# Kernel tuning notes

Measured on AMD Instinct MI355X. Metric: run time of the kernel, lower is better.

The kernel has to match this reference:

```python
import jax, jax.numpy as jnp
import numpy as np

H = 16  # n_heads

def setup_inputs() -> dict:
    key = jax.random.key(0)
    k1, k2, k3, k4 = jax.random.split(key, 4)
    B, S, D = 2, 2048, 1024
    query = jax.random.normal(k1, (B, S, D), dtype=jnp.float32)
    pos_emb = jax.random.normal(k2, (S, D), dtype=jnp.float32)
    w_qkv = jax.random.normal(k3, (D, 3 * D), dtype=jnp.float32) * (D ** -0.5)
    w_out = jax.random.normal(k4, (D, D), dtype=jnp.float32) * (D ** -0.5)
    return {"query": query, "pos_emb": pos_emb, "w_qkv": w_qkv, "w_out": w_out}

def reference(query, pos_emb, w_qkv, w_out):
    B, S, D = query.shape
    d_k = D // H
    # ape=True: pos_fn applied to input before QKV projection (additive APE)
    x = query + pos_emb[None, :, :]
    # fused QKV projection; torch view(B,S,H,3*d_k) + chunk(3,-1) == reshape(B,S,H,3,d_k)
    qkv = jnp.einsum('bsd,de->bse', x, w_qkv).reshape(B, S, H, 3, d_k)
    qkv = jnp.transpose(qkv, (0, 2, 1, 3, 4))  # [B,H,S,3,d_k]
    q, k, v = qkv[..., 0, :], qkv[..., 1, :], qkv[..., 2, :]
    scale = d_k ** -0.5
    scores = jnp.einsum('bhqd,bhkd->bhqk', q, k) * scale  # [B,H,S,S]
    attn = jax.nn.softmax(scores, axis=-1)  # dropout is identity in eval
    o = jnp.einsum('bhqk,bhkd->bhqd', attn, v)
    o = jnp.transpose(o, (0, 2, 1, 3)).reshape(B, S, D)
    return jnp.einsum('bsd,de->bse', o, w_out)
```

## Files before the change

kernel.cpp:

```cpp
#include <hip/hip_runtime.h>

#define SS 2048
#define DD 1024
#define N3 3072

typedef unsigned short u16;
typedef unsigned int u32;
typedef __attribute__((ext_vector_type(8))) short bf16x8;
typedef __attribute__((ext_vector_type(4))) short bf16x4;
typedef __attribute__((ext_vector_type(4))) float f32x4;

__device__ __forceinline__ u16 f2bf(float f) {
    u32 u = __float_as_uint(f);
    u32 r = u + 0x7fffu + ((u >> 16) & 1u);
    return (u16)(r >> 16);
}

__device__ __forceinline__ float fast_exp2(float x) {
    return __builtin_amdgcn_exp2f(x);
}

__device__ __forceinline__ void async_cp16(u16* lds, const u16* g) {
    __builtin_amdgcn_global_load_lds((const __attribute__((address_space(1))) u32*)g,
                                     (__attribute__((address_space(3))) u32*)lds, 16, 0, 0);
}

__device__ __forceinline__ f32x4 mfma16(bf16x4 a, bf16x4 b, f32x4 c) {
    return __builtin_amdgcn_mfma_f32_16x16x16bf16_1k(a, b, c, 0, 0, 0);
}

__global__ __launch_bounds__(256)
void prep_all(const float* __restrict__ q, const float* __restrict__ pos,
              const float* __restrict__ wqkv, const float* __restrict__ wout,
              u16* __restrict__ x, u16* __restrict__ wqkvT, u16* __restrict__ woutT)
{
    __shared__ float t[32][33];
    const int bx = blockIdx.x;

    if (bx < 4096) {
        const size_t i = ((size_t)bx * 256 + threadIdx.x) * 4;
        float4 a = *(const float4*)(q + i);
        float4 p = *(const float4*)(pos + (i & (size_t)(SS * DD - 1)));
        uint2 r;
        r.x = (u32)f2bf(a.x + p.x) | ((u32)f2bf(a.y + p.y) << 16);
        r.y = (u32)f2bf(a.z + p.z) | ((u32)f2bf(a.w + p.w) << 16);
        *(uint2*)(x + i) = r;
        return;
    }

    const int isq = bx < 7168;
    const int tt  = isq ? (bx - 4096) : (bx - 7168);
    const int nx  = isq ? 96 : 32;
    const int N   = isq ? N3 : DD;
    const float* W = isq ? wqkv : wout;
    u16* WT = isq ? wqkvT : woutT;

    const int x0 = (tt % nx) * 32, y0 = (tt / nx) * 32;
    const int tx = threadIdx.x & 31, ty = threadIdx.x >> 5;
#pragma unroll
    for (int i = 0; i < 4; ++i)
        t[ty + i * 8][tx] = W[(size_t)(y0 + ty + i * 8) * N + x0 + tx];
    __syncthreads();
#pragma unroll
    for (int i = 0; i < 4; ++i) {
        const int n = x0 + ty + i * 8;
        int dst = n;
        if (isq) {
            const int hh = n / 192, r = n % 192;
            dst = (r < 64) ? hh * 64 + r
                : (r < 128) ? 1024 + hh * 64 + (r - 64)
                            : 2048 + hh * 64 + (r - 128);
        }
        float v = t[tx][ty + i * 8];
        if (isq && dst < 1024) v *= 0.18033688f;
        WT[(size_t)dst * DD + y0 + tx] = f2bf(v);
    }
}

__global__ __launch_bounds__(512, 2)
void gemm256(const u16* __restrict__ A, const u16* __restrict__ BT,
             u16* __restrict__ C, u16* __restrict__ vt, int M, int N, int K, int nbx)
{
    extern __shared__ __align__(16) u16 smem[];

    const int bid = blockIdx.x;
    const int chunk = (int)gridDim.x >> 3;
    const int swz = (bid & 7) * chunk + (bid >> 3);
    const int bxs = swz % nbx, bys = swz / nbx;

    const int tid = threadIdx.x;
    const int lane = tid & 63;
    const int wv = tid >> 6;
    const int quad = lane >> 4, l16 = lane & 15;
    const int wm = wv >> 2, wn = wv & 3;
    const int m0 = bys * 256, n0 = bxs * 256;
    const int sw = l16 & 7;

    const int srow = tid >> 3, pc = tid & 7, lc = pc ^ (srow & 7);
    const u16* agp = A  + (size_t)(m0 + srow) * K + lc * 8;
    const u16* bgp = BT + (size_t)(n0 + srow) * K + lc * 8;
    u16* const asw = smem +         srow * 64 + pc * 8;
    u16* const bsw = smem + 32768 + srow * 64 + pc * 8;

    auto stage = [&](int buf, int k0) {
#pragma unroll
        for (int s = 0; s < 4; ++s)
            async_cp16(asw + buf * 16384 + s * 4096, agp + (size_t)(s * 64) * K + k0);
#pragma unroll
        for (int s = 0; s < 4; ++s)
            async_cp16(bsw + buf * 16384 + s * 4096, bgp + (size_t)(s * 64) * K + k0);
    };

    f32x4 acc[8][4];
#pragma unroll
    for (int i = 0; i < 8; ++i)
#pragma unroll
        for (int j = 0; j < 4; ++j) acc[i][j] = {0.f, 0.f, 0.f, 0.f};

    stage(0, 0);

    const int NT = K / 64;
    for (int t = 0; t < NT; ++t) {
        const int p = t & 1;
        asm volatile("s_waitcnt vmcnt(0) lgkmcnt(0)\n\ts_barrier" ::: "memory");
        if (t + 1 < NT) stage(p ^ 1, (t + 1) * 64);

        const u16* Ab = smem +         p * 16384;
        const u16* Bb = smem + 32768 + p * 16384;

#pragma unroll
        for (int ks = 0; ks < 2; ++ks) {
            bf16x8 bfr[4];
#pragma unroll
            for (int nt = 0; nt < 4; ++nt)
                bfr[nt] = *(const bf16x8*)&Bb[(wn * 64 + nt * 16 + l16) * 64 + (((ks * 4 + quad) ^ sw) << 3)];
#pragma unroll
            for (int mt = 0; mt < 8; ++mt) {
                bf16x8 af = *(const bf16x8*)&Ab[(wm * 128 + mt * 16 + l16) * 64 + (((ks * 4 + quad) ^ sw) << 3)];
#pragma unroll
                for (int nt = 0; nt < 4; ++nt)
                    acc[mt][nt] = __builtin_amdgcn_mfma_f32_16x16x32_bf16(af, bfr[nt], acc[mt][nt], 0, 0, 0);
            }
        }
    }

    if (vt && n0 >= 2048) {
        __syncthreads();
        u16* tb = smem;
#pragma unroll
        for (int mt = 0; mt < 8; ++mt)
#pragma unroll
            for (int nt = 0; nt < 4; ++nt) {
                const int vl = wn * 64 + nt * 16 + l16;
                const int ml = wm * 128 + mt * 16 + quad * 4;
                uint2 w;
                w.x = (u32)f2bf(acc[mt][nt][0]) | ((u32)f2bf(acc[mt][nt][1]) << 16);
                w.y = (u32)f2bf(acc[mt][nt][2]) | ((u32)f2bf(acc[mt][nt][3]) << 16);
                *(uint2*)(tb + (size_t)vl * 264 + ml) = w;
            }
        __syncthreads();
        const int vl = tid >> 1, half = tid & 1;
        const int b16 = (m0 >> 11) * 16;
        const int hh = ((n0 - 2048) >> 6) + (vl >> 6);
        const int dk = vl & 63;
        u16* dst = vt + ((size_t)(b16 + hh) * 64 + dk) * SS + (m0 & 2047) + half * 128;
        const u16* src = tb + (size_t)vl * 264 + half * 128;
#pragma unroll
        for (int j = 0; j < 16; ++j)
            *(uint4*)(dst + j * 8) = *(const uint4*)(src + j * 8);
    } else {
#pragma unroll
        for (int mt = 0; mt < 8; ++mt)
#pragma unroll
            for (int r = 0; r < 4; ++r) {
                const size_t row = m0 + wm * 128 + mt * 16 + quad * 4 + r;
                u16* cp = C + row * N + n0 + wn * 64 + l16;
#pragma unroll
                for (int nt = 0; nt < 4; ++nt) cp[nt * 16] = f2bf(acc[mt][nt][r]);
            }
    }
}

template <int OUT_BF16, int NT>
__global__ __launch_bounds__(256)
void gemm_mfma(const u16* __restrict__ A, const u16* __restrict__ BT,
               void* __restrict__ Cv, int M, int N, int K, int nbx)
{
    constexpr int FR = NT / 32;
    __shared__ u16 As[2][128 * 64];
    __shared__ u16 Bs[2][NT * 64];

    const int bid = blockIdx.x;
    const int chunk = (int)gridDim.x >> 3;
    const int swz = (bid & 7) * chunk + (bid >> 3);
    const int bxs = swz % nbx, bys = swz / nbx;

    const int tid = threadIdx.x;
    const int lane = tid & 63, wv = tid >> 6;
    const int quad = lane >> 4, l16 = lane & 15;
    const int m0 = bys * 128, n0 = bxs * NT;

    const int arow = wv * 32 + (lane >> 3);
    const int pc   = lane & 7;
    const int lcA  = pc ^ (arow & 7);
    const u16* agp = A + (size_t)(m0 + arow) * K + lcA * 8;

    const int brow = (NT == 128) ? (wv * 32 + (lane >> 3)) : (wv * 8 + (lane >> 3));
    const int lcB  = pc ^ (brow & 7);
    const u16* bgp = BT + (size_t)(n0 + brow) * K + lcB * 8;

    const int aoff = arow * 64 + pc * 8;
    const int boff = brow * 64 + pc * 8;

    auto stage = [&](int buf, int k0) {
#pragma unroll
        for (int s = 0; s < 4; ++s)
            async_cp16(&As[buf][aoff + s * 8 * 64], agp + (size_t)(s * 8) * K + k0);
        if constexpr (NT == 128) {
#pragma unroll
            for (int s = 0; s < 4; ++s)
                async_cp16(&Bs[buf][boff + s * 8 * 64], bgp + (size_t)(s * 8) * K + k0);
        } else {
#pragma unroll
            for (int s = 0; s < 2; ++s)
                async_cp16(&Bs[buf][boff + s * 32 * 64], bgp + (size_t)(s * 32) * K + k0);
        }
    };

    const int moff = (wv >> 1) * 64, noff = (wv & 1) * (NT / 2);

    f32x4 acc[4][FR];
#pragma unroll
    for (int i = 0; i < 4; ++i)
#pragma unroll
        for (int j = 0; j < FR; ++j) acc[i][j] = {0.f, 0.f, 0.f, 0.f};

    const int swf = l16 & 7;

    stage(0, 0);

    const int NTILES = K / 64;
    for (int t = 0; t < NTILES; ++t) {
        const int p = t & 1;
        asm volatile("s_waitcnt vmcnt(0) lgkmcnt(0)\n\ts_barrier" ::: "memory");
        if (t + 1 < NTILES) stage(p ^ 1, (t + 1) * 64);

        const u16* Ab = As[p];
        const u16* Bb = Bs[p];

#pragma unroll
        for (int ks = 0; ks < 2; ++ks) {
            bf16x8 af[4], bfr[FR];
#pragma unroll
            for (int tt = 0; tt < 4; ++tt)
                af[tt] = *(const bf16x8*)&Ab[(moff + tt * 16 + l16) * 64 + (((ks * 4 + quad) ^ swf) << 3)];
#pragma unroll
            for (int tt = 0; tt < FR; ++tt)
                bfr[tt] = *(const bf16x8*)&Bb[(noff + tt * 16 + l16) * 64 + (((ks * 4 + quad) ^ swf) << 3)];
#pragma unroll
            for (int mt = 0; mt < 4; ++mt)
#pragma unroll
                for (int nt = 0; nt < FR; ++nt)
                    acc[mt][nt] = __builtin_amdgcn_mfma_f32_16x16x32_bf16(af[mt], bfr[nt], acc[mt][nt], 0, 0, 0);
        }
    }

#pragma unroll
    for (int mt = 0; mt < 4; ++mt)
#pragma unroll
        for (int r = 0; r < 4; ++r) {
            const size_t row = m0 + moff + mt * 16 + quad * 4 + r;
            if (OUT_BF16) {
                u16* cp = (u16*)Cv + row * N + n0 + noff + l16;
#pragma unroll
                for (int nt = 0; nt < FR; ++nt) cp[nt * 16] = f2bf(acc[mt][nt][r]);
            } else {
                float* cp = (float*)Cv + row * N + n0 + noff + l16;
#pragma unroll
                for (int nt = 0; nt < FR; ++nt) cp[nt * 16] = acc[mt][nt][r];
            }
        }
}

__global__ __launch_bounds__(512, 4)
void attn_mfma(const u16* __restrict__ qkv, const u16* __restrict__ vt, u16* __restrict__ o)
{
    __shared__ __align__(16) u16 smem[32768];

    const int tid = threadIdx.x;
    const int lane = tid & 63, wv = tid >> 6;
    const int grp = wv >> 2, w4 = wv & 3;
    const int quad = lane >> 4, l16 = lane & 15;
    const int bx = blockIdx.x;
    const int bh = bx & 31, qt = bx >> 5;
    const int h = bh & 15, b = bh >> 4;

    const size_t base = (size_t)b * SS * N3;
    const int q0 = qt * 128 + w4 * 32;
    const int sw = l16 & 7;

    bf16x8 qf[2][2];
#pragma unroll
    for (int mt = 0; mt < 2; ++mt)
#pragma unroll
        for (int ks = 0; ks < 2; ++ks)
            qf[mt][ks] = *(const bf16x8*)(qkv + base + h * 64 + (size_t)(q0 + mt * 16 + l16) * N3 + ks * 32 + quad * 8);

    f32x4 po[2][4];
#pragma unroll
    for (int mt = 0; mt < 2; ++mt)
#pragma unroll
        for (int nt = 0; nt < 4; ++nt) po[mt][nt] = {0.f, 0.f, 0.f, 0.f};
    float lrun[2] = {0.f, 0.f};

    const int lrow = lane >> 3, pc8 = lane & 7, lc = pc8 ^ lrow;
    const int srow = w4 * 16;
    const int kt0 = grp * 16;

    const u16* kgp = qkv + base + 1024 + h * 64 + (size_t)(kt0 * 64 + srow + lrow) * N3 + lc * 8;
    const u16* vgp = vt + ((size_t)bh * 64 + srow + lrow) * SS + kt0 * 64 + lc * 8;

    u16* const ksA = smem + (grp * 2) * 4096 + (srow + lrow) * 64 + pc8 * 8;
    u16* const ksB = ksA + 4096;
    u16* const vsA = smem + 16384 + (grp * 2) * 4096 + (srow + lrow) * 64 + pc8 * 8;
    u16* const vsB = vsA + 4096;

    async_cp16(ksA,       kgp);
    async_cp16(ksA + 512, kgp + (size_t)8 * N3);
    async_cp16(vsA,       vgp);
    async_cp16(vsA + 512, vgp + (size_t)8 * SS);

    for (int it = 0; it < 16; ++it) {
        const int p = it & 1;
        asm volatile("s_waitcnt vmcnt(0) lgkmcnt(0)\n\ts_barrier" ::: "memory");
        if (it < 15) {
            const size_t ko = (size_t)(it + 1) * 64;
            u16* kb = p ? ksA : ksB;
            u16* vb = p ? vsA : vsB;
            async_cp16(kb,       kgp + ko * N3);
            async_cp16(kb + 512, kgp + ko * N3 + (size_t)8 * N3);
            async_cp16(vb,       vgp + ko);
            async_cp16(vb + 512, vgp + ko + (size_t)8 * SS);
        }
        const u16* kbuf = smem + (grp * 2 + p) * 4096;
        const u16* vbuf = smem + 16384 + (grp * 2 + p) * 4096;

        f32x4 sf[2][4];
#pragma unroll
        for (int mt = 0; mt < 2; ++mt)
#pragma unroll
            for (int kn = 0; kn < 4; ++kn) sf[mt][kn] = {0.f, 0.f, 0.f, 0.f};
        __builtin_amdgcn_s_setprio(1);
#pragma unroll
        for (int ks = 0; ks < 2; ++ks)
#pragma unroll
            for (int kn = 0; kn < 4; ++kn) {
                bf16x8 kf = *(const bf16x8*)&kbuf[(kn * 16 + l16) * 64 + (((ks * 4 + quad) ^ sw) << 3)];
#pragma unroll
                for (int mt = 0; mt < 2; ++mt)
                    sf[mt][kn] = __builtin_amdgcn_mfma_f32_16x16x32_bf16(kf, qf[mt][ks], sf[mt][kn], 0, 0, 0);
            }
        __builtin_amdgcn_s_setprio(0);

        __builtin_amdgcn_s_setprio(1);
#pragma unroll
        for (int kn = 0; kn < 4; ++kn) {
            bf16x4 vf[4];
#pragma unroll
            for (int nt = 0; nt < 4; ++nt)
                vf[nt] = *(const bf16x4*)&vbuf[(nt * 16 + l16) * 64 + (((2 * kn + (quad >> 1)) ^ sw) << 3) + ((quad & 1) << 2)];
#pragma unroll
            for (int mt = 0; mt < 2; ++mt) {
                const float p0 = fast_exp2(sf[mt][kn][0]);
                const float p1 = fast_exp2(sf[mt][kn][1]);
                const float p2 = fast_exp2(sf[mt][kn][2]);
                const float p3 = fast_exp2(sf[mt][kn][3]);
                lrun[mt] += (p0 + p1) + (p2 + p3);
                union { bf16x4 v; u32 w[2]; } pu;
                pu.w[0] = __builtin_amdgcn_perm(__float_as_uint(p1), __float_as_uint(p0), 0x07060302u);
                pu.w[1] = __builtin_amdgcn_perm(__float_as_uint(p3), __float_as_uint(p2), 0x07060302u);
#pragma unroll
                for (int nt = 0; nt < 4; ++nt)
                    po[mt][nt] = mfma16(vf[nt], pu.v, po[mt][nt]);
            }
        }
        __builtin_amdgcn_s_setprio(0);
    }

    __syncthreads();

#pragma unroll
    for (int mt = 0; mt < 2; ++mt) {
        lrun[mt] += __shfl_xor(lrun[mt], 16, 64);
        lrun[mt] += __shfl_xor(lrun[mt], 32, 64);
    }

    float* xch = (float*)smem;
    if (grp == 1) {
        float* d = xch + (w4 * 64 + lane) * 36;
#pragma unroll
        for (int mt = 0; mt < 2; ++mt)
#pragma unroll
            for (int nt = 0; nt < 4; ++nt)
                *(f32x4*)(d + mt * 16 + nt * 4) = po[mt][nt];
        d[32] = lrun[0]; d[33] = lrun[1];
    }
    __syncthreads();
    if (grp == 0) {
        const float* s = xch + (w4 * 64 + lane) * 36;
#pragma unroll
        for (int mt = 0; mt < 2; ++mt)
#pragma unroll
            for (int nt = 0; nt < 4; ++nt)
                po[mt][nt] = po[mt][nt] + *(const f32x4*)(s + mt * 16 + nt * 4);
        lrun[0] += s[32]; lrun[1] += s[33];

#pragma unroll
        for (int mt = 0; mt < 2; ++mt) {
            const float linv = 1.f / lrun[mt];
            const size_t row = (size_t)b * SS + q0 + mt * 16 + l16;
#pragma unroll
            for (int nt = 0; nt < 4; ++nt) {
                const u32 h0 = (u32)f2bf(po[mt][nt][0] * linv) | ((u32)f2bf(po[mt][nt][1] * linv) << 16);
                const u32 h1 = (u32)f2bf(po[mt][nt][2] * linv) | ((u32)f2bf(po[mt][nt][3] * linv) << 16);
                uint2 wp; wp.x = h0; wp.y = h1;
                *(uint2*)(o + row * DD + h * 64 + nt * 16 + quad * 4) = wp;
            }
        }
    }
}

extern "C" void kernel_launch(void* const* d_in, const int* in_sizes, int n_in,
                              void* d_out, int out_size, void* d_ws, size_t ws_size,
                              hipStream_t stream)
{
    const float* query  = (const float*)d_in[0];
    const float* posemb = (const float*)d_in[1];
    const float* w_qkv  = (const float*)d_in[2];
    const float* w_out  = (const float*)d_in[3];
    float* out = (float*)d_out;

    u16* xb    = (u16*)d_ws;
    u16* wqkvT = xb    + (size_t)4096 * 1024;
    u16* woutT = wqkvT + (size_t)3072 * 1024;
    u16* qkv   = woutT + (size_t)1024 * 1024;
    u16* ob    = qkv   + (size_t)4096 * 3072;
    u16* vtb   = ob    + (size_t)4096 * 1024;

    static bool lds_init = false;
    if (!lds_init) {
        hipFuncSetAttribute((const void*)gemm256,
                            hipFuncAttributeMaxDynamicSharedMemorySize, 135168);
        lds_init = true;
    }

    prep_all<<<8192, 256, 0, stream>>>(query, posemb, w_qkv, w_out, xb, wqkvT, woutT);

    gemm256<<<192, 512, 135168, stream>>>(xb, wqkvT, qkv, vtb, 4096, N3, DD, N3 / 256);

    attn_mfma<<<dim3(512, 1, 1), 512, 0, stream>>>(qkv, vtb, ob);

    gemm_mfma<0, 64><<<512, 256, 0, stream>>>(ob, woutT, (void*)out, 4096, DD, DD, DD / 64);
}
```

Before: 179.1 us.

## Read V fragments directly from global memory and halve attention LDS footprint

Stops staging the transposed V tiles through shared memory and has each lane load its bf16x4 V fragments straight from global/L2 inside the PV loop. This halves the attention kernel's LDS allocation, and the final cross-group reduction is split into two passes to fit the smaller buffer. The aim is to reduce LDS pressure so more blocks fit per CU. In exchange, V reads become narrow 8-byte strided global loads on the critical path with no async prefetch, which adds latency and uses memory bandwidth less efficiently.

```diff
diff --git a/kernel.cpp b/kernel.cpp
--- a/kernel.cpp
+++ b/kernel.cpp
@@ -285,7 +285,7 @@
 __global__ __launch_bounds__(512, 4)
 void attn_mfma(const u16* __restrict__ qkv, const u16* __restrict__ vt, u16* __restrict__ o)
 {
-    __shared__ __align__(16) u16 smem[32768];
+    __shared__ __align__(16) u16 smem[16384];
 
     const int tid = threadIdx.x;
     const int lane = tid & 63, wv = tid >> 6;
@@ -318,17 +318,14 @@
     const int kt0 = grp * 16;
 
     const u16* kgp = qkv + base + 1024 + h * 64 + (size_t)(kt0 * 64 + srow + lrow) * N3 + lc * 8;
-    const u16* vgp = vt + ((size_t)bh * 64 + srow + lrow) * SS + kt0 * 64 + lc * 8;
+
+    const u16* vbase = vt + ((size_t)bh * 64 + l16) * SS + grp * 1024 + quad * 4;
 
     u16* const ksA = smem + (grp * 2) * 4096 + (srow + lrow) * 64 + pc8 * 8;
     u16* const ksB = ksA + 4096;
-    u16* const vsA = smem + 16384 + (grp * 2) * 4096 + (srow + lrow) * 64 + pc8 * 8;
-    u16* const vsB = vsA + 4096;
 
     async_cp16(ksA,       kgp);
     async_cp16(ksA + 512, kgp + (size_t)8 * N3);
-    async_cp16(vsA,       vgp);
-    async_cp16(vsA + 512, vgp + (size_t)8 * SS);
 
     for (int it = 0; it < 16; ++it) {
         const int p = it & 1;
@@ -336,14 +333,11 @@
         if (it < 15) {
             const size_t ko = (size_t)(it + 1) * 64;
             u16* kb = p ? ksA : ksB;
-            u16* vb = p ? vsA : vsB;
             async_cp16(kb,       kgp + ko * N3);
             async_cp16(kb + 512, kgp + ko * N3 + (size_t)8 * N3);
-            async_cp16(vb,       vgp + ko);
-            async_cp16(vb + 512, vgp + ko + (size_t)8 * SS);
         }
         const u16* kbuf = smem + (grp * 2 + p) * 4096;
-        const u16* vbuf = smem + 16384 + (grp * 2 + p) * 4096;
+        const u16* vit = vbase + it * 64;
 
         f32x4 sf[2][4];
 #pragma unroll
@@ -368,7 +362,7 @@
             bf16x4 vf[4];
 #pragma unroll
             for (int nt = 0; nt < 4; ++nt)
-                vf[nt] = *(const bf16x4*)&vbuf[(nt * 16 + l16) * 64 + (((2 * kn + (quad >> 1)) ^ sw) << 3) + ((quad & 1) << 2)];
+                vf[nt] = *(const bf16x4*)(vit + (size_t)(nt * 16) * SS + kn * 16);
 #pragma unroll
             for (int mt = 0; mt < 2; ++mt) {
                 const float p0 = fast_exp2(sf[mt][kn][0]);
@@ -397,23 +391,31 @@
 
     float* xch = (float*)smem;
     if (grp == 1) {
-        float* d = xch + (w4 * 64 + lane) * 36;
-#pragma unroll
-        for (int mt = 0; mt < 2; ++mt)
-#pragma unroll
-            for (int nt = 0; nt < 4; ++nt)
-                *(f32x4*)(d + mt * 16 + nt * 4) = po[mt][nt];
-        d[32] = lrun[0]; d[33] = lrun[1];
+        float* d = xch + (w4 * 64 + lane) * 16;
+#pragma unroll
+        for (int nt = 0; nt < 4; ++nt) *(f32x4*)(d + nt * 4) = po[0][nt];
     }
     __syncthreads();
     if (grp == 0) {
-        const float* s = xch + (w4 * 64 + lane) * 36;
-#pragma unroll
-        for (int mt = 0; mt < 2; ++mt)
-#pragma unroll
-            for (int nt = 0; nt < 4; ++nt)
-                po[mt][nt] = po[mt][nt] + *(const f32x4*)(s + mt * 16 + nt * 4);
-        lrun[0] += s[32]; lrun[1] += s[33];
+        const float* s = xch + (w4 * 64 + lane) * 16;
+#pragma unroll
+        for (int nt = 0; nt < 4; ++nt) po[0][nt] = po[0][nt] + *(const f32x4*)(s + nt * 4);
+    }
+    __syncthreads();
+    if (grp == 1) {
+        float* d = xch + (w4 * 64 + lane) * 16;
+#pragma unroll
+        for (int nt = 0; nt < 4; ++nt) *(f32x4*)(d + nt * 4) = po[1][nt];
+        float* d2 = xch + 4096 + (w4 * 64 + lane) * 2;
+        d2[0] = lrun[0]; d2[1] = lrun[1];
+    }
+    __syncthreads();
+    if (grp == 0) {
+        const float* s = xch + (w4 * 64 + lane) * 16;
+#pragma unroll
+        for (int nt = 0; nt < 4; ++nt) po[1][nt] = po[1][nt] + *(const f32x4*)(s + nt * 4);
+        const float* s2 = xch + 4096 + (w4 * 64 + lane) * 2;
+        lrun[0] += s2[0]; lrun[1] += s2[1];
 
 #pragma unroll
         for (int mt = 0; mt < 2; ++mt) {
```

Measured after the change: 261.9 us. +46.2%, slower.
